# Optimization experiments

Measured on AMD Instinct MI355X. Metric: run time of the kernel, lower is better.

## Reference

```python
import jax, jax.numpy as jnp
import numpy as np

B, N, F, FH, H = 8, 2048, 64, 64, 4
NEG_BIG = -1e10


def setup_inputs() -> dict:
    key = jax.random.key(0)
    k_x, k_a, k_w, k_as, k_an = jax.random.split(key, 5)
    X = jax.random.normal(k_x, (B, N, F), dtype=jnp.float32)
    A = (jax.random.uniform(k_a, (B, N, N)) < 0.1).astype(jnp.float32)
    A = jnp.maximum(A, jnp.eye(N, dtype=jnp.float32)[None])
    W = jax.random.normal(k_w, (H, F, FH), dtype=jnp.float32) * (1.0 / np.sqrt(F))
    b = jnp.zeros((H, FH), dtype=jnp.float32)
    a_self = jax.random.normal(k_as, (H, FH), dtype=jnp.float32) * (1.0 / np.sqrt(FH))
    a_neigh = jax.random.normal(k_an, (H, FH), dtype=jnp.float32) * (1.0 / np.sqrt(FH))
    return {"X": X, "A": A, "W": W, "b": b, "a_self": a_self, "a_neigh": a_neigh}


def reference(X, A, W, b, a_self, a_neigh):
    # per-head linear projection: [B,H,N,FH]
    feats = jnp.einsum("bnf,hfo->bhno", X, W)
    # additive attention logits: e_ij = leaky_relu(a_s.h_i + a_n.h_j)
    s_self = jnp.einsum("bhno,ho->bhn", feats, a_self)   # [B,H,N]
    s_neigh = jnp.einsum("bhno,ho->bhn", feats, a_neigh)  # [B,H,N]
    scores = s_self[:, :, :, None] + s_neigh[:, :, None, :]  # [B,H,N,N]
    scores = jax.nn.leaky_relu(scores, negative_slope=0.2)
    scores = scores + (1.0 - A)[:, None] * NEG_BIG  # adjacency mask
    attn = jax.nn.softmax(scores, axis=-1)
    # weighted aggregation + bias (dropouts are identity at inference)
    out = jnp.einsum("bhnm,bhmo->bhno", attn, feats) + b[None, :, None, :]
    # concat heads -> [B,N,H*FH], then activation
    Bd, Hd, Nd, Fd = out.shape
    out = jnp.transpose(out, (0, 2, 1, 3)).reshape(Bd, Nd, Hd * Fd)
    return jax.nn.relu(out)
```

## Files before the change

kernel.cpp:

```cpp
#include <hip/hip_runtime.h>
#include <hip/hip_bf16.h>
#include <stdint.h>

#define B_ 8
#define N_ 2048
#define F_ 64
#define FH_ 64
#define H_ 4
#define C_ (H_*FH_)
#define LOG2E 1.44269504088896340736f

typedef short short8 __attribute__((ext_vector_type(8)));
typedef float f32x4 __attribute__((ext_vector_type(4)));

__device__ __forceinline__ short f2bf(float f) {
    __hip_bfloat16 h = __float2bfloat16(f);
    return __builtin_bit_cast(short, h);
}

__global__ __launch_bounds__(256) void k0_wt(const float* __restrict__ W,
                                             __hip_bfloat16* __restrict__ WT) {
    int idx = blockIdx.x * 256 + threadIdx.x;
    int h = idx >> 12, rem = idx & 4095, o = rem >> 6, f = rem & 63;
    WT[idx] = __float2bfloat16(W[(h * F_ + f) * FH_ + o]);
}

__global__ __launch_bounds__(256) void k1_feats(const float* __restrict__ X,
                                                const __hip_bfloat16* __restrict__ WT,
                                                __hip_bfloat16* __restrict__ featsT) {
    const int nb = blockIdx.x, h = blockIdx.y, b = blockIdx.z;
    const int wave = threadIdx.x >> 6, lane = threadIdx.x & 63;
    const int m = lane & 15, q = lane >> 4;
    const int n = nb * 64 + wave * 16 + m;
    f32x4 acc[4] = {};
#pragma unroll
    for (int ks = 0; ks < 2; ++ks) {
        const float* xp = X + ((size_t)(b * N_ + n)) * F_ + ks * 32 + q * 8;
        float4 x0 = *(const float4*)xp;
        float4 x1 = *(const float4*)(xp + 4);
        short8 bfrag;
        bfrag[0] = f2bf(x0.x); bfrag[1] = f2bf(x0.y);
        bfrag[2] = f2bf(x0.z); bfrag[3] = f2bf(x0.w);
        bfrag[4] = f2bf(x1.x); bfrag[5] = f2bf(x1.y);
        bfrag[6] = f2bf(x1.z); bfrag[7] = f2bf(x1.w);
#pragma unroll
        for (int ot = 0; ot < 4; ++ot) {
            short8 afrag = *(const short8*)(WT + ((size_t)(h * FH_ + ot * 16 + m)) * F_ + ks * 32 + q * 8);
            acc[ot] = __builtin_amdgcn_mfma_f32_16x16x32_bf16(afrag, bfrag, acc[ot], 0, 0, 0);
        }
    }
#pragma unroll
    for (int ot = 0; ot < 4; ++ot) {
#pragma unroll
        for (int r = 0; r < 4; ++r) {
            int orow = ot * 16 + q * 4 + r;
            featsT[((size_t)(b * H_ + h) * FH_ + orow) * N_ + n] = __float2bfloat16(acc[ot][r]);
        }
    }
}

__global__ __launch_bounds__(256) void k2_scores(const float* __restrict__ X,
                                                 const float* __restrict__ W,
                                                 const float* __restrict__ a_self,
                                                 const float* __restrict__ a_neigh,
                                                 float* __restrict__ ss, float* __restrict__ sn) {
    __shared__ float wl[2][H_][F_];
    const int tid = threadIdx.x;
    {
        int h = tid >> 6, f = tid & 63;
        float as_ = 0.f, an_ = 0.f;
#pragma unroll
        for (int o = 0; o < FH_; ++o) {
            float w = W[(h * F_ + f) * FH_ + o];
            as_ += w * a_self[h * FH_ + o];
            an_ += w * a_neigh[h * FH_ + o];
        }
        wl[0][h][f] = as_;
        wl[1][h][f] = an_;
    }
    __syncthreads();
    const int b = blockIdx.x >> 3;
    const int n = (blockIdx.x & 7) * 256 + tid;
    float xr[F_];
#pragma unroll
    for (int f = 0; f < F_; ++f) xr[f] = X[((size_t)(b * N_ + n)) * F_ + f];
#pragma unroll
    for (int h = 0; h < H_; ++h) {
        float ds = 0.f, dn = 0.f;
#pragma unroll
        for (int f = 0; f < F_; ++f) {
            ds += xr[f] * wl[0][h][f];
            dn += xr[f] * wl[1][h][f];
        }
        ss[((size_t)(b * H_ + h)) * N_ + n] = ds * LOG2E;
        sn[((size_t)(b * H_ + h)) * N_ + n] = dn * LOG2E;
    }
}

__global__ __launch_bounds__(256) void k3_attn(const float* __restrict__ A,
                                               const __hip_bfloat16* __restrict__ featsT,
                                               const float* __restrict__ ss,
                                               const float* __restrict__ sn,
                                               const float* __restrict__ bias,
                                               float* __restrict__ out) {
    __shared__ float sn_lds[H_ * N_];
    const int bx = blockIdx.x;
    const int b = bx >> 6;
    const int itile = bx & 63;
    const int tid = threadIdx.x;
    const int h = tid >> 6;
    const int lane = tid & 63;
    const int m = lane & 15, q = lane >> 4;
    const int ibase = itile * 32;

    {
        const float4* src = (const float4*)(sn + ((size_t)(b * H_ + h)) * N_);
        float4* dst = (float4*)(sn_lds + h * N_);
#pragma unroll
        for (int i = 0; i < 8; ++i) dst[lane + i * 64] = src[lane + i * 64];
    }
    const float ss0 = ss[((size_t)(b * H_ + h)) * N_ + ibase + m];
    const float ss1 = ss[((size_t)(b * H_ + h)) * N_ + ibase + 16 + m];
    __syncthreads();

    const float* arow0 = A + ((size_t)(b * N_ + ibase + m)) * N_ + q * 8;
    const float* arow1 = arow0 + (size_t)16 * N_;
    const __hip_bfloat16* fb = featsT + (((size_t)(b * H_ + h)) * FH_ + m) * N_ + q * 8;
    const float* snh = sn_lds + h * N_ + q * 8;

    f32x4 acc[2][4] = {};
    float l0 = 0.f, l1 = 0.f;

#pragma unroll 2
    for (int jb = 0; jb < N_; jb += 32) {
        float4 sv0 = *(const float4*)(snh + jb);
        float4 sv1 = *(const float4*)(snh + jb + 4);
        float4 a00 = *(const float4*)(arow0 + jb);
        float4 a01 = *(const float4*)(arow0 + jb + 4);
        float4 a10 = *(const float4*)(arow1 + jb);
        float4 a11 = *(const float4*)(arow1 + jb + 4);
        float snv[8] = {sv0.x, sv0.y, sv0.z, sv0.w, sv1.x, sv1.y, sv1.z, sv1.w};
        float ma[8]  = {a00.x, a00.y, a00.z, a00.w, a01.x, a01.y, a01.z, a01.w};
        float mb[8]  = {a10.x, a10.y, a10.z, a10.w, a11.x, a11.y, a11.z, a11.w};
        short8 p0, p1;
#pragma unroll
        for (int s = 0; s < 8; ++s) {
            float t0 = ss0 + snv[s];
            float t1 = ss1 + snv[s];
            float pa = ma[s] * exp2f(fmaxf(t0, 0.2f * t0));
            float pb = mb[s] * exp2f(fmaxf(t1, 0.2f * t1));
            p0[s] = f2bf(pa);
            p1[s] = f2bf(pb);
            l0 += pa;
            l1 += pb;
        }
#pragma unroll
        for (int ct = 0; ct < 4; ++ct) {
            short8 fv = *(const short8*)(fb + (size_t)ct * 16 * N_ + jb);
            acc[0][ct] = __builtin_amdgcn_mfma_f32_16x16x32_bf16(p0, fv, acc[0][ct], 0, 0, 0);
            acc[1][ct] = __builtin_amdgcn_mfma_f32_16x16x32_bf16(p1, fv, acc[1][ct], 0, 0, 0);
        }
    }

    l0 += __shfl_xor(l0, 16); l0 += __shfl_xor(l0, 32);
    l1 += __shfl_xor(l1, 16); l1 += __shfl_xor(l1, 32);

    float bc[4];
#pragma unroll
    for (int ct = 0; ct < 4; ++ct) bc[ct] = bias[h * FH_ + ct * 16 + m];

#pragma unroll
    for (int sub = 0; sub < 2; ++sub) {
        float lsub = sub ? l1 : l0;
#pragma unroll
        for (int r = 0; r < 4; ++r) {
            int row_local = q * 4 + r;
            float lv = __shfl(lsub, row_local);
            float inv = 1.0f / lv;
            int gr = ibase + sub * 16 + row_local;
#pragma unroll
            for (int ct = 0; ct < 4; ++ct) {
                float v = acc[sub][ct][r] * inv + bc[ct];
                out[((size_t)b * N_ + gr) * C_ + h * FH_ + ct * 16 + m] = fmaxf(v, 0.0f);
            }
        }
    }
}

extern "C" void kernel_launch(void* const* d_in, const int* in_sizes, int n_in,
                              void* d_out, int out_size, void* d_ws, size_t ws_size,
                              hipStream_t stream) {
    const float* X       = (const float*)d_in[0];
    const float* A       = (const float*)d_in[1];
    const float* W       = (const float*)d_in[2];
    const float* bias    = (const float*)d_in[3];
    const float* a_self  = (const float*)d_in[4];
    const float* a_neigh = (const float*)d_in[5];
    float* out = (float*)d_out;

    char* ws = (char*)d_ws;
    __hip_bfloat16* featsT = (__hip_bfloat16*)(ws);
    __hip_bfloat16* WT     = (__hip_bfloat16*)(ws + 8388608);
    float* ss              = (float*)(ws + 8421376);
    float* sn              = (float*)(ws + 8683520);

    k0_wt    <<<64, 256, 0, stream>>>(W, WT);
    k1_feats <<<dim3(N_ / 64, H_, B_), 256, 0, stream>>>(X, WT, featsT);
    k2_scores<<<B_ * N_ / 256, 256, 0, stream>>>(X, W, a_self, a_neigh, ss, sn);
    k3_attn  <<<B_ * (N_ / 32), 256, 0, stream>>>(A, featsT, ss, sn, bias, out);
}
```

Baseline: 307.7 us.

## Factor attention exponentials, fuse score projection into feats, compute row sums via MFMA

```diff
diff --git a/kernel.cpp b/kernel.cpp
--- a/kernel.cpp
+++ b/kernel.cpp
@@ -27,9 +27,19 @@
 
 __global__ __launch_bounds__(256) void k1_feats(const float* __restrict__ X,
                                                 const __hip_bfloat16* __restrict__ WT,
-                                                __hip_bfloat16* __restrict__ featsT) {
+                                                const float* __restrict__ a_self,
+                                                const float* __restrict__ a_neigh,
+                                                __hip_bfloat16* __restrict__ featsT,
+                                                float* __restrict__ ss,
+                                                float* __restrict__ sn) {
+    __shared__ float a_lds[2][FH_];
     const int nb = blockIdx.x, h = blockIdx.y, b = blockIdx.z;
-    const int wave = threadIdx.x >> 6, lane = threadIdx.x & 63;
+    const int tid = threadIdx.x;
+    if (tid < 64)       a_lds[0][tid] = a_self[h * FH_ + tid];
+    else if (tid < 128) a_lds[1][tid - 64] = a_neigh[h * FH_ + tid - 64];
+    __syncthreads();
+
+    const int wave = tid >> 6, lane = tid & 63;
     const int m = lane & 15, q = lane >> 4;
     const int n = nb * 64 + wave * 16 + m;
     f32x4 acc[4] = {};
@@ -49,51 +59,23 @@
             acc[ot] = __builtin_amdgcn_mfma_f32_16x16x32_bf16(afrag, bfrag, acc[ot], 0, 0, 0);
         }
     }
+    float ssv = 0.f, snv = 0.f;
 #pragma unroll
     for (int ot = 0; ot < 4; ++ot) {
 #pragma unroll
         for (int r = 0; r < 4; ++r) {
             int orow = ot * 16 + q * 4 + r;
-            featsT[((size_t)(b * H_ + h) * FH_ + orow) * N_ + n] = __float2bfloat16(acc[ot][r]);
+            float v = acc[ot][r];
+            featsT[((size_t)(b * H_ + h) * FH_ + orow) * N_ + n] = __float2bfloat16(v);
+            ssv += v * a_lds[0][orow];
+            snv += v * a_lds[1][orow];
         }
     }
-}
-
-__global__ __launch_bounds__(256) void k2_scores(const float* __restrict__ X,
-                                                 const float* __restrict__ W,
-                                                 const float* __restrict__ a_self,
-                                                 const float* __restrict__ a_neigh,
-                                                 float* __restrict__ ss, float* __restrict__ sn) {
-    __shared__ float wl[2][H_][F_];
-    const int tid = threadIdx.x;
-    {
-        int h = tid >> 6, f = tid & 63;
-        float as_ = 0.f, an_ = 0.f;
-#pragma unroll
-        for (int o = 0; o < FH_; ++o) {
-            float w = W[(h * F_ + f) * FH_ + o];
-            as_ += w * a_self[h * FH_ + o];
-            an_ += w * a_neigh[h * FH_ + o];
-        }
-        wl[0][h][f] = as_;
-        wl[1][h][f] = an_;
-    }
-    __syncthreads();
-    const int b = blockIdx.x >> 3;
-    const int n = (blockIdx.x & 7) * 256 + tid;
-    float xr[F_];
-#pragma unroll
-    for (int f = 0; f < F_; ++f) xr[f] = X[((size_t)(b * N_ + n)) * F_ + f];
-#pragma unroll
-    for (int h = 0; h < H_; ++h) {
-        float ds = 0.f, dn = 0.f;
-#pragma unroll
-        for (int f = 0; f < F_; ++f) {
-            ds += xr[f] * wl[0][h][f];
-            dn += xr[f] * wl[1][h][f];
-        }
-        ss[((size_t)(b * H_ + h)) * N_ + n] = ds * LOG2E;
-        sn[((size_t)(b * H_ + h)) * N_ + n] = dn * LOG2E;
+    ssv += __shfl_xor(ssv, 16); ssv += __shfl_xor(ssv, 32);
+    snv += __shfl_xor(snv, 16); snv += __shfl_xor(snv, 32);
+    if (lane < 16) {
+        ss[((size_t)(b * H_ + h)) * N_ + n] = ssv * LOG2E;
+        sn[((size_t)(b * H_ + h)) * N_ + n] = snv * LOG2E;
     }
 }
 
@@ -103,86 +85,82 @@
                                                const float* __restrict__ sn,
                                                const float* __restrict__ bias,
                                                float* __restrict__ out) {
-    __shared__ float sn_lds[H_ * N_];
-    const int bx = blockIdx.x;
-    const int b = bx >> 6;
-    const int itile = bx & 63;
-    const int tid = threadIdx.x;
-    const int h = tid >> 6;
-    const int lane = tid & 63;
+    __shared__ float e1_lds[N_];
+    __shared__ float e2_lds[N_];
+    const int tile = blockIdx.x, h = blockIdx.y, b = blockIdx.z;
+    const int tid = threadIdx.x, wave = tid >> 6, lane = tid & 63;
     const int m = lane & 15, q = lane >> 4;
-    const int ibase = itile * 32;
 
     {
-        const float4* src = (const float4*)(sn + ((size_t)(b * H_ + h)) * N_);
-        float4* dst = (float4*)(sn_lds + h * N_);
+        const float4* snrow = (const float4*)(sn + ((size_t)(b * H_ + h)) * N_);
+        float4* e1v = (float4*)e1_lds;
+        float4* e2v = (float4*)e2_lds;
 #pragma unroll
-        for (int i = 0; i < 8; ++i) dst[lane + i * 64] = src[lane + i * 64];
+        for (int i = 0; i < 2; ++i) {
+            int idx = tid + i * 256;
+            float4 v = snrow[idx];
+            float4 u1, u2;
+            u1.x = exp2f(v.x); u1.y = exp2f(v.y); u1.z = exp2f(v.z); u1.w = exp2f(v.w);
+            u2.x = exp2f(0.2f * v.x); u2.y = exp2f(0.2f * v.y);
+            u2.z = exp2f(0.2f * v.z); u2.w = exp2f(0.2f * v.w);
+            e1v[idx] = u1; e2v[idx] = u2;
+        }
     }
-    const float ss0 = ss[((size_t)(b * H_ + h)) * N_ + ibase + m];
-    const float ss1 = ss[((size_t)(b * H_ + h)) * N_ + ibase + 16 + m];
+    const int rowbase = tile * 64 + wave * 16;
+    const float ss0 = ss[((size_t)(b * H_ + h)) * N_ + rowbase + m];
+    const float e1i = exp2f(ss0), e2i = exp2f(0.2f * ss0);
     __syncthreads();
 
-    const float* arow0 = A + ((size_t)(b * N_ + ibase + m)) * N_ + q * 8;
-    const float* arow1 = arow0 + (size_t)16 * N_;
+    const float* arow = A + ((size_t)(b * N_ + rowbase + m)) * N_ + q * 8;
     const __hip_bfloat16* fb = featsT + (((size_t)(b * H_ + h)) * FH_ + m) * N_ + q * 8;
-    const float* snh = sn_lds + h * N_ + q * 8;
+    const float* p1 = e1_lds + q * 8;
+    const float* p2 = e2_lds + q * 8;
 
-    f32x4 acc[2][4] = {};
-    float l0 = 0.f, l1 = 0.f;
+    f32x4 acc[4] = {};
+    f32x4 accl = {};
+    short8 ones;
+#pragma unroll
+    for (int s = 0; s < 8; ++s) ones[s] = (short)0x3F80;
 
 #pragma unroll 2
     for (int jb = 0; jb < N_; jb += 32) {
-        float4 sv0 = *(const float4*)(snh + jb);
-        float4 sv1 = *(const float4*)(snh + jb + 4);
-        float4 a00 = *(const float4*)(arow0 + jb);
-        float4 a01 = *(const float4*)(arow0 + jb + 4);
-        float4 a10 = *(const float4*)(arow1 + jb);
-        float4 a11 = *(const float4*)(arow1 + jb + 4);
-        float snv[8] = {sv0.x, sv0.y, sv0.z, sv0.w, sv1.x, sv1.y, sv1.z, sv1.w};
-        float ma[8]  = {a00.x, a00.y, a00.z, a00.w, a01.x, a01.y, a01.z, a01.w};
-        float mb[8]  = {a10.x, a10.y, a10.z, a10.w, a11.x, a11.y, a11.z, a11.w};
-        short8 p0, p1;
+        float4 ea0 = *(const float4*)(p1 + jb);
+        float4 ea1 = *(const float4*)(p1 + jb + 4);
+        float4 eb0 = *(const float4*)(p2 + jb);
+        float4 eb1 = *(const float4*)(p2 + jb + 4);
+        float4 m0  = *(const float4*)(arow + jb);
+        float4 m1  = *(const float4*)(arow + jb + 4);
+        float e1a[8] = {ea0.x, ea0.y, ea0.z, ea0.w, ea1.x, ea1.y, ea1.z, ea1.w};
+        float e2a[8] = {eb0.x, eb0.y, eb0.z, eb0.w, eb1.x, eb1.y, eb1.z, eb1.w};
+        float mk[8]  = {m0.x, m0.y, m0.z, m0.w, m1.x, m1.y, m1.z, m1.w};
+        short8 p;
 #pragma unroll
         for (int s = 0; s < 8; ++s) {
-            float t0 = ss0 + snv[s];
-            float t1 = ss1 + snv[s];
-            float pa = ma[s] * exp2f(fmaxf(t0, 0.2f * t0));
-            float pb = mb[s] * exp2f(fmaxf(t1, 0.2f * t1));
-            p0[s] = f2bf(pa);
-            p1[s] = f2bf(pb);
-            l0 += pa;
-            l1 += pb;
+            float hi = e1i * e1a[s];
+            float lo = e2i * e2a[s];
+            float v = (hi > 1.0f) ? hi : lo;
+            p[s] = f2bf(mk[s] * v);
         }
 #pragma unroll
         for (int ct = 0; ct < 4; ++ct) {
-            short8 fv = *(const short8*)(fb + (size_t)ct * 16 * N_ + jb);
-            acc[0][ct] = __builtin_amdgcn_mfma_f32_16x16x32_bf16(p0, fv, acc[0][ct], 0, 0, 0);
-            acc[1][ct] = __builtin_amdgcn_mfma_f32_16x16x32_bf16(p1, fv, acc[1][ct], 0, 0, 0);
+            short8 fv = *(const short8*)(fb + (size_t)(ct * 16) * N_ + jb);
+            acc[ct] = __builtin_amdgcn_mfma_f32_16x16x32_bf16(p, fv, acc[ct], 0, 0, 0);
         }
+        accl = __builtin_amdgcn_mfma_f32_16x16x32_bf16(p, ones, accl, 0, 0, 0);
     }
-
-    l0 += __shfl_xor(l0, 16); l0 += __shfl_xor(l0, 32);
-    l1 += __shfl_xor(l1, 16); l1 += __shfl_xor(l1, 32);
 
     float bc[4];
 #pragma unroll
     for (int ct = 0; ct < 4; ++ct) bc[ct] = bias[h * FH_ + ct * 16 + m];
 
 #pragma unroll
-    for (int sub = 0; sub < 2; ++sub) {
-        float lsub = sub ? l1 : l0;
+    for (int r = 0; r < 4; ++r) {
+        float inv = 1.0f / accl[r];
+        int gr = rowbase + q * 4 + r;
 #pragma unroll
-        for (int r = 0; r < 4; ++r) {
-            int row_local = q * 4 + r;
-            float lv = __shfl(lsub, row_local);
-            float inv = 1.0f / lv;
-            int gr = ibase + sub * 16 + row_local;
-#pragma unroll
-            for (int ct = 0; ct < 4; ++ct) {
-                float v = acc[sub][ct][r] * inv + bc[ct];
-                out[((size_t)b * N_ + gr) * C_ + h * FH_ + ct * 16 + m] = fmaxf(v, 0.0f);
-            }
+        for (int ct = 0; ct < 4; ++ct) {
+            float v = acc[ct][r] * inv + bc[ct];
+            out[((size_t)(b * N_) + gr) * C_ + h * FH_ + ct * 16 + m] = fmaxf(v, 0.0f);
         }
     }
 }
@@ -205,7 +183,6 @@
     float* sn              = (float*)(ws + 8683520);
 
     k0_wt    <<<64, 256, 0, stream>>>(W, WT);
-    k1_feats <<<dim3(N_ / 64, H_, B_), 256, 0, stream>>>(X, WT, featsT);
-    k2_scores<<<B_ * N_ / 256, 256, 0, stream>>>(X, W, a_self, a_neigh, ss, sn);
-    k3_attn  <<<B_ * (N_ / 32), 256, 0, stream>>>(A, featsT, ss, sn, bias, out);
+    k1_feats <<<dim3(N_ / 64, H_, B_), 256, 0, stream>>>(X, WT, a_self, a_neigh, featsT, ss, sn);
+    k3_attn  <<<dim3(N_ / 64, H_, B_), 256, 0, stream>>>(A, featsT, ss, sn, bias, out);
 }
```

After: 345.4 us. +12.3%, slower.
